# Performance work log

Hardware: AMD Instinct MI355X
Metric: run time of the kernel (lower is better)

Reference implementation:

```python
import jax, jax.numpy as jnp
import numpy as np

B, D, H, K = 32768, 784, 500, 50


def setup_inputs() -> dict:
    key = jax.random.key(0)
    ks = jax.random.split(key, 12)
    s = 0.02  # weight init scale
    return {
        "x": jax.random.uniform(ks[0], (B, D), dtype=jnp.float32),
        "u": jax.random.uniform(ks[1], (B, K), dtype=jnp.float32),
        "enc_w1": jax.random.normal(ks[2], (D, H), dtype=jnp.float32) * s,
        "enc_b1": jnp.zeros((H,), jnp.float32),
        "w_alpha": jax.random.normal(ks[3], (H, K), dtype=jnp.float32) * s,
        "b_alpha": jnp.zeros((K,), jnp.float32),
        "w_beta": jax.random.normal(ks[4], (H, K), dtype=jnp.float32) * s,
        "b_beta": jnp.zeros((K,), jnp.float32),
        "dec_w1": jax.random.normal(ks[5], (K, H), dtype=jnp.float32) * s,
        "dec_b1": jnp.zeros((H,), jnp.float32),
        "dec_w2": jax.random.normal(ks[6], (H, D), dtype=jnp.float32) * s,
        "dec_b2": jnp.zeros((D,), jnp.float32),
    }


def reference(x, u, enc_w1, enc_b1, w_alpha, b_alpha, w_beta, b_beta,
              dec_w1, dec_b1, dec_w2, dec_b2):
    # encode
    h = jax.nn.relu(x @ enc_w1 + enc_b1)                       # [B,H]
    alpha = jax.nn.softplus(h @ w_alpha + b_alpha)             # [B,K] > 0
    beta = jax.nn.softplus(h @ w_beta + b_beta)                # [B,K] > 0
    # Kumaraswamy inverse-CDF sample: v = (1 - u^(1/beta))^(1/alpha)
    v = (1.0 - u ** (1.0 / beta)) ** (1.0 / alpha)             # [B,K]
    # stick-breaking: pi[k] = v[k] * prod_{j<k}(1 - v[j])  (exclusive cumprod)
    cp = jnp.cumprod(1.0 - v, axis=-1)                         # [B,K]
    pi = v * jnp.concatenate([jnp.ones_like(v[:, :1]), cp[:, :-1]], axis=-1)
    # decode
    hd = jax.nn.relu(pi @ dec_w1 + dec_b1)                     # [B,H]
    recon_x = jax.nn.sigmoid(hd @ dec_w2 + dec_b2)             # [B,D]
    return recon_x, alpha, beta
```

## Files before the change

### kernel.cpp

```cpp
#include <hip/hip_runtime.h>
#include <math.h>


typedef __bf16 bf16x8 __attribute__((ext_vector_type(8)));
typedef float f32x4 __attribute__((ext_vector_type(4)));

#define BATCH 32768
#define BM 128
#define BN 128
#define BK 64
#define NTHR 512

__device__ __forceinline__ unsigned short bf16_bits(float f) {
    __bf16 b = (__bf16)f;
    return __builtin_bit_cast(unsigned short, b);
}

__device__ __forceinline__ void gll16(const void* src, void* ldsdst) {
    __builtin_amdgcn_global_load_lds(
        (const __attribute__((address_space(1))) unsigned int*)src,
        (__attribute__((address_space(3))) unsigned int*)ldsdst,
        16, 0, 0);
}

template<int MODE>
__global__ __launch_bounds__(NTHR, 4) void mfma_gemm(
    const unsigned short* __restrict__ A,
    const unsigned short* __restrict__ Bt,
    const float* __restrict__ bias,
    void* __restrict__ Cv,
    int Kpad, int lda, int ldc, int Nreal, int nbx)
{
    __shared__ unsigned short As[BM * BK];
    __shared__ unsigned short Bs[BN * BK];

    const int nwg = gridDim.x;
    const int orig = blockIdx.x;
    const int q = nwg >> 3, r8 = nwg & 7;
    const int xcd = orig & 7;
    const int chunkbase = (xcd < r8) ? xcd * (q + 1) : r8 * (q + 1) + (xcd - r8) * q;
    const int wgid = chunkbase + (orig >> 3);
    const int bn = wgid % nbx;
    const size_t block_m = (size_t)(wgid / nbx) * BM;
    const int block_n = bn * BN;

    const int tid = threadIdx.x;
    const int l = tid & 63;
    const int wid = tid >> 6;
    const int wr = wid >> 2, wc = wid & 3;

    const int lr = l & 15;
    const int kh = l >> 4;

    f32x4 acc[4][2] = {};

    for (int k0 = 0; k0 < Kpad; k0 += BK) {
        #pragma unroll
        for (int i = 0; i < 2; ++i) {
            int chunk = wid * 2 + i;
            int gid = chunk * 64 + l;
            int r = gid >> 3;
            int kgs = (gid & 7) ^ (r & 7);
            gll16(Bt + (size_t)(block_n + r) * Kpad + k0 + kgs * 8, Bs + chunk * 512);
        }
        #pragma unroll
        for (int i = 0; i < 2; ++i) {
            int chunk = wid * 2 + i;
            int gid = chunk * 64 + l;
            int r = gid >> 3;
            int kgs = (gid & 7) ^ (r & 7);
            gll16(A + (block_m + r) * (size_t)lda + k0 + kgs * 8, As + chunk * 512);
        }
        __syncthreads();

        #pragma unroll
        for (int s = 0; s < 2; ++s) {
            bf16x8 af[4], bf[2];
            #pragma unroll
            for (int mi = 0; mi < 4; ++mi) {
                int row = wr * 64 + mi * 16 + lr;
                int g = (s * 4 + kh) ^ (row & 7);
                af[mi] = *(const bf16x8*)(As + row * 64 + g * 8);
            }
            #pragma unroll
            for (int ni = 0; ni < 2; ++ni) {
                int row = wc * 32 + ni * 16 + lr;
                int g = (s * 4 + kh) ^ (row & 7);
                bf[ni] = *(const bf16x8*)(Bs + row * 64 + g * 8);
            }
            #pragma unroll
            for (int mi = 0; mi < 4; ++mi)
                #pragma unroll
                for (int ni = 0; ni < 2; ++ni)
                    acc[mi][ni] = __builtin_amdgcn_mfma_f32_16x16x32_bf16(
                        af[mi], bf[ni], acc[mi][ni], 0, 0, 0);
        }
        __syncthreads();
    }

    const int rg = (l >> 4) * 4;
    #pragma unroll
    for (int mi = 0; mi < 4; ++mi) {
        #pragma unroll
        for (int ni = 0; ni < 2; ++ni) {
            int gn = block_n + wc * 32 + ni * 16 + lr;
            float bs = bias[gn];
            #pragma unroll
            for (int j = 0; j < 4; ++j) {
                long gm = block_m + wr * 64 + mi * 16 + rg + j;
                float z = acc[mi][ni][j] + bs;
                if (MODE == 0) {
                    z = fmaxf(z, 0.f);
                    ((unsigned short*)Cv)[gm * ldc + gn] = bf16_bits(z);
                } else if (MODE == 1) {
                    z = (z > 0.f) ? z + __logf(1.f + __expf(-z))
                                  : __logf(1.f + __expf(z));
                    float* out = (float*)Cv;
                    if (gn < 50)       out[gm * 50 + gn] = z;
                    else if (gn < 100) out[(size_t)BATCH * 50 + gm * 50 + (gn - 50)] = z;
                } else {
                    if (gn < Nreal) {
                        z = __fdividef(1.f, 1.f + __expf(-z));
                        ((float*)Cv)[gm * Nreal + gn] = z;
                    }
                }
            }
        }
    }
}

__global__ __launch_bounds__(256) void cast_x(
    const float* __restrict__ x, unsigned short* __restrict__ xb)
{
    int gid = blockIdx.x * 256 + threadIdx.x;
    int r = gid / 104;
    int c = gid - r * 104;
    union { __bf16 b[8]; uint4 u; } pk;
    if (c < 98) {
        const float4* p = (const float4*)(x + (size_t)r * 784 + c * 8);
        float4 f0 = p[0], f1 = p[1];
        pk.b[0] = (__bf16)f0.x; pk.b[1] = (__bf16)f0.y;
        pk.b[2] = (__bf16)f0.z; pk.b[3] = (__bf16)f0.w;
        pk.b[4] = (__bf16)f1.x; pk.b[5] = (__bf16)f1.y;
        pk.b[6] = (__bf16)f1.z; pk.b[7] = (__bf16)f1.w;
    } else {
        pk.u = make_uint4(0, 0, 0, 0);
    }
    *(uint4*)(xb + (size_t)r * 832 + c * 8) = pk.u;
}

__global__ __launch_bounds__(256) void prep_bt(
    const float* __restrict__ W, const float* __restrict__ bias,
    unsigned short* __restrict__ Bt, float* __restrict__ bpad,
    int Kr, int Nr, int Kpad, int Npad)
{
    int idx = blockIdx.x * 256 + threadIdx.x;
    if (idx >= Npad * Kpad) return;
    int n = idx / Kpad, k = idx - n * Kpad;
    float v = (n < Nr && k < Kr) ? W[(size_t)k * Nr + n] : 0.f;
    Bt[idx] = bf16_bits(v);
    if (k == 0) bpad[n] = (n < Nr) ? bias[n] : 0.f;
}

__global__ __launch_bounds__(256) void prep_wab(
    const float* __restrict__ Wa, const float* __restrict__ Wb,
    const float* __restrict__ ba, const float* __restrict__ bb,
    unsigned short* __restrict__ Bt, float* __restrict__ bpad)
{
    int idx = blockIdx.x * 256 + threadIdx.x;
    if (idx >= 128 * 512) return;
    int n = idx >> 9, k = idx & 511;
    float v = 0.f;
    if (k < 500) {
        if (n < 50)       v = Wa[(size_t)k * 50 + n];
        else if (n < 100) v = Wb[(size_t)k * 50 + (n - 50)];
    }
    Bt[idx] = bf16_bits(v);
    if (k == 0) bpad[n] = (n < 50) ? ba[n] : ((n < 100) ? bb[n - 50] : 0.f);
}

__global__ __launch_bounds__(256) void sample_pi(
    const float* __restrict__ u, const float* __restrict__ alpha,
    const float* __restrict__ beta, unsigned short* __restrict__ pib)
{
    int row = (blockIdx.x * 256 + threadIdx.x) >> 6;
    int lane = threadIdx.x & 63;
    size_t base = (size_t)row * 50;

    float v = 0.f, w = 1.f;
    if (lane < 50) {
        float a = alpha[base + lane];
        float b = beta[base + lane];
        float uu = u[base + lane];
        float t = exp2f(__fdividef(log2f(uu), b));
        v = exp2f(__fdividef(log2f(1.f - t), a));
        w = 1.f - v;
    }
    float p = w;
    #pragma unroll
    for (int off = 1; off < 64; off <<= 1) {
        float t = __shfl_up(p, off, 64);
        if (lane >= off) p *= t;
    }
    float ex = __shfl_up(p, 1, 64);
    if (lane == 0) ex = 1.f;
    float pi = v * ex;
    pib[(size_t)row * 64 + lane] = (lane < 50) ? bf16_bits(pi) : (unsigned short)0;
}

extern "C" void kernel_launch(void* const* d_in, const int* in_sizes, int n_in,
                              void* d_out, int out_size, void* d_ws, size_t ws_size,
                              hipStream_t stream) {
    const float* x       = (const float*)d_in[0];
    const float* u       = (const float*)d_in[1];
    const float* enc_w1  = (const float*)d_in[2];
    const float* enc_b1  = (const float*)d_in[3];
    const float* w_alpha = (const float*)d_in[4];
    const float* b_alpha = (const float*)d_in[5];
    const float* w_beta  = (const float*)d_in[6];
    const float* b_beta  = (const float*)d_in[7];
    const float* dec_w1  = (const float*)d_in[8];
    const float* dec_b1  = (const float*)d_in[9];
    const float* dec_w2  = (const float*)d_in[10];
    const float* dec_b2  = (const float*)d_in[11];

    const int D = 784;

    float* out   = (float*)d_out;
    float* recon = out;
    float* alpha = out + (size_t)BATCH * D;

    unsigned short* xb = (unsigned short*)d_out;

    char* ws = (char*)d_ws;
    unsigned short* w1b  = (unsigned short*)(ws);
    unsigned short* wab  = (unsigned short*)(ws + 851968);
    unsigned short* dw1b = (unsigned short*)(ws + 983040);
    unsigned short* dw2b = (unsigned short*)(ws + 1048576);
    float* bias1  = (float*)(ws + 1966080);
    float* biasab = (float*)(ws + 1968128);
    float* biasd1 = (float*)(ws + 1970688);
    float* biasd2 = (float*)(ws + 1972736);
    unsigned short* h    = (unsigned short*)(ws + 2097152);
    unsigned short* pib  = (unsigned short*)(ws + 35651584);
    unsigned short* hdb  = h;

    cast_x<<<dim3(BATCH * 104 / 256), 256, 0, stream>>>(x, xb);
    prep_bt<<<dim3(512 * 832 / 256), 256, 0, stream>>>(
        enc_w1, enc_b1, w1b, bias1, 784, 500, 832, 512);
    prep_wab<<<dim3(256), 256, 0, stream>>>(w_alpha, w_beta, b_alpha, b_beta, wab, biasab);
    prep_bt<<<dim3(512 * 64 / 256), 256, 0, stream>>>(
        dec_w1, dec_b1, dw1b, biasd1, 50, 500, 64, 512);
    prep_bt<<<dim3(896 * 512 / 256), 256, 0, stream>>>(
        dec_w2, dec_b2, dw2b, biasd2, 500, 784, 512, 896);

    mfma_gemm<0><<<dim3((512 / BN) * (BATCH / BM)), NTHR, 0, stream>>>(
        xb, w1b, bias1, h, 832, 832, 512, 500, 512 / BN);

    mfma_gemm<1><<<dim3(BATCH / BM), NTHR, 0, stream>>>(
        h, wab, biasab, alpha, 512, 512, 0, 100, 1);

    sample_pi<<<dim3(BATCH * 64 / 256), 256, 0, stream>>>(
        u, alpha, alpha + (size_t)BATCH * 50, pib);

    mfma_gemm<0><<<dim3((512 / BN) * (BATCH / BM)), NTHR, 0, stream>>>(
        pib, dw1b, biasd1, hdb, 64, 64, 512, 500, 512 / BN);

    mfma_gemm<2><<<dim3((896 / BN) * (BATCH / BM)), NTHR, 0, stream>>>(
        hdb, dw2b, biasd2, recon, 512, 512, 784, 784, 896 / BN);
}
```

Measured before the change: 153.1 us.

## Fuse stick-breaking sampling into decoder first GEMM and merge weight-prep kernels

Adds a kernel that computes the Kumaraswamy samples and stick-breaking pi for a 128-row tile directly into LDS, then runs the 50→500 decoder GEMM with MFMA from that LDS tile. Weight tiles are double-buffered through global_load_lds. This removes the pi round-trip through global memory and one kernel launch, and each block now covers all 512 output columns instead of computing pi once per column block. The four weight-prep launches are also merged into one kernel with block-range dispatch. The cost is a serial sampling phase of 16 rows per wave before any MFMA work starts, plus scattered 2-byte stores of hdb.

```diff
diff --git a/kernel.cpp b/kernel.cpp
--- a/kernel.cpp
+++ b/kernel.cpp
@@ -129,6 +129,115 @@
     }
 }
 
+__global__ __launch_bounds__(NTHR, 4) void sample_gemm4(
+    const float* __restrict__ u, const float* __restrict__ alpha,
+    const float* __restrict__ beta,
+    const unsigned short* __restrict__ dw1b,
+    const float* __restrict__ biasd1,
+    unsigned short* __restrict__ hdb)
+{
+    __shared__ unsigned short Pi[128 * 64];
+    __shared__ unsigned short Wd[2][128 * 64];
+
+    const int tid = threadIdx.x;
+    const int l = tid & 63;
+    const int wid = tid >> 6;
+
+    const int nwg = gridDim.x;
+    const int orig = blockIdx.x;
+    const int q = nwg >> 3, r8 = nwg & 7;
+    const int xcd = orig & 7;
+    const int chunkbase = (xcd < r8) ? xcd * (q + 1) : r8 * (q + 1) + (xcd - r8) * q;
+    const int wgid = chunkbase + (orig >> 3);
+    const size_t block_m = (size_t)wgid * 128;
+
+    auto stageW = [&](int j, int buf) {
+        #pragma unroll
+        for (int i = 0; i < 2; ++i) {
+            int chunk = wid * 2 + i;
+            int gid = chunk * 64 + l;
+            int r = gid >> 3;
+            int kgs = (gid & 7) ^ (r & 7);
+            gll16(dw1b + (size_t)(j * 128 + r) * 64 + kgs * 8,
+                  &Wd[buf][chunk * 512]);
+        }
+    };
+
+    stageW(0, 0);
+
+    for (int rr = 0; rr < 16; ++rr) {
+        int row = wid * 16 + rr;
+        size_t grow = block_m + row;
+        float v = 0.f, w = 1.f;
+        if (l < 50) {
+            float a = alpha[grow * 50 + l];
+            float b = beta[grow * 50 + l];
+            float uu = u[grow * 50 + l];
+            float t = exp2f(__fdividef(log2f(uu), b));
+            v = exp2f(__fdividef(log2f(1.f - t), a));
+            w = 1.f - v;
+        }
+        float p = w;
+        #pragma unroll
+        for (int off = 1; off < 64; off <<= 1) {
+            float t2 = __shfl_up(p, off, 64);
+            if (l >= off) p *= t2;
+        }
+        float ex = __shfl_up(p, 1, 64);
+        if (l == 0) ex = 1.f;
+        float pi = (l < 50) ? v * ex : 0.f;
+        Pi[row * 64 + (((l >> 3) ^ (row & 7)) << 3) + (l & 7)] = bf16_bits(pi);
+    }
+    __syncthreads();
+
+    const int lr = l & 15, kh = l >> 4;
+    const int wr = wid >> 2, wc = wid & 3;
+    const int rg = (l >> 4) * 4;
+
+    for (int j = 0; j < 4; ++j) {
+        if (j < 3) stageW(j + 1, (j + 1) & 1);
+        f32x4 acc[4][2] = {};
+        const unsigned short* W = Wd[j & 1];
+        #pragma unroll
+        for (int s = 0; s < 2; ++s) {
+            bf16x8 af[4], bf[2];
+            #pragma unroll
+            for (int mi = 0; mi < 4; ++mi) {
+                int row = wr * 64 + mi * 16 + lr;
+                int g = (s * 4 + kh) ^ (row & 7);
+                af[mi] = *(const bf16x8*)(Pi + row * 64 + g * 8);
+            }
+            #pragma unroll
+            for (int ni = 0; ni < 2; ++ni) {
+                int row = wc * 32 + ni * 16 + lr;
+                int g = (s * 4 + kh) ^ (row & 7);
+                bf[ni] = *(const bf16x8*)(W + row * 64 + g * 8);
+            }
+            #pragma unroll
+            for (int mi = 0; mi < 4; ++mi)
+                #pragma unroll
+                for (int ni = 0; ni < 2; ++ni)
+                    acc[mi][ni] = __builtin_amdgcn_mfma_f32_16x16x32_bf16(
+                        af[mi], bf[ni], acc[mi][ni], 0, 0, 0);
+        }
+        #pragma unroll
+        for (int mi = 0; mi < 4; ++mi) {
+            #pragma unroll
+            for (int ni = 0; ni < 2; ++ni) {
+                int gn = j * 128 + wc * 32 + ni * 16 + lr;
+                float bs = biasd1[gn];
+                #pragma unroll
+                for (int jj = 0; jj < 4; ++jj) {
+                    long gm = block_m + wr * 64 + mi * 16 + rg + jj;
+                    float z = fmaxf(acc[mi][ni][jj] + bs, 0.f);
+                    hdb[gm * 512 + gn] = bf16_bits(z);
+                }
+            }
+        }
+        __syncthreads();
+    }
+}
+
 __global__ __launch_bounds__(256) void cast_x(
     const float* __restrict__ x, unsigned short* __restrict__ xb)
 {
@@ -149,63 +258,48 @@
     *(uint4*)(xb + (size_t)r * 832 + c * 8) = pk.u;
 }
 
-__global__ __launch_bounds__(256) void prep_bt(
-    const float* __restrict__ W, const float* __restrict__ bias,
-    unsigned short* __restrict__ Bt, float* __restrict__ bpad,
-    int Kr, int Nr, int Kpad, int Npad)
+__global__ __launch_bounds__(256) void prep_all(
+    const float* __restrict__ enc_w1, const float* __restrict__ enc_b1,
+    const float* __restrict__ Wa, const float* __restrict__ ba,
+    const float* __restrict__ Wb, const float* __restrict__ bb,
+    const float* __restrict__ dec_w1, const float* __restrict__ dec_b1,
+    const float* __restrict__ dec_w2, const float* __restrict__ dec_b2,
+    unsigned short* __restrict__ w1b, float* __restrict__ bias1,
+    unsigned short* __restrict__ wab, float* __restrict__ biasab,
+    unsigned short* __restrict__ dw1b, float* __restrict__ biasd1,
+    unsigned short* __restrict__ dw2b, float* __restrict__ biasd2)
 {
-    int idx = blockIdx.x * 256 + threadIdx.x;
-    if (idx >= Npad * Kpad) return;
-    int n = idx / Kpad, k = idx - n * Kpad;
-    float v = (n < Nr && k < Kr) ? W[(size_t)k * Nr + n] : 0.f;
-    Bt[idx] = bf16_bits(v);
-    if (k == 0) bpad[n] = (n < Nr) ? bias[n] : 0.f;
-}
-
-__global__ __launch_bounds__(256) void prep_wab(
-    const float* __restrict__ Wa, const float* __restrict__ Wb,
-    const float* __restrict__ ba, const float* __restrict__ bb,
-    unsigned short* __restrict__ Bt, float* __restrict__ bpad)
-{
-    int idx = blockIdx.x * 256 + threadIdx.x;
-    if (idx >= 128 * 512) return;
-    int n = idx >> 9, k = idx & 511;
-    float v = 0.f;
-    if (k < 500) {
-        if (n < 50)       v = Wa[(size_t)k * 50 + n];
-        else if (n < 100) v = Wb[(size_t)k * 50 + (n - 50)];
-    }
-    Bt[idx] = bf16_bits(v);
-    if (k == 0) bpad[n] = (n < 50) ? ba[n] : ((n < 100) ? bb[n - 50] : 0.f);
-}
-
-__global__ __launch_bounds__(256) void sample_pi(
-    const float* __restrict__ u, const float* __restrict__ alpha,
-    const float* __restrict__ beta, unsigned short* __restrict__ pib)
-{
-    int row = (blockIdx.x * 256 + threadIdx.x) >> 6;
-    int lane = threadIdx.x & 63;
-    size_t base = (size_t)row * 50;
-
-    float v = 0.f, w = 1.f;
-    if (lane < 50) {
-        float a = alpha[base + lane];
-        float b = beta[base + lane];
-        float uu = u[base + lane];
-        float t = exp2f(__fdividef(log2f(uu), b));
-        v = exp2f(__fdividef(log2f(1.f - t), a));
-        w = 1.f - v;
-    }
-    float p = w;
-    #pragma unroll
-    for (int off = 1; off < 64; off <<= 1) {
-        float t = __shfl_up(p, off, 64);
-        if (lane >= off) p *= t;
-    }
-    float ex = __shfl_up(p, 1, 64);
-    if (lane == 0) ex = 1.f;
-    float pi = v * ex;
-    pib[(size_t)row * 64 + lane] = (lane < 50) ? bf16_bits(pi) : (unsigned short)0;
+    int bid = blockIdx.x;
+    int t = threadIdx.x;
+    if (bid < 1664) {
+        int idx = bid * 256 + t;
+        int n = idx / 832, k = idx - n * 832;
+        float v = (n < 500 && k < 784) ? enc_w1[(size_t)k * 500 + n] : 0.f;
+        w1b[idx] = bf16_bits(v);
+        if (k == 0) bias1[n] = (n < 500) ? enc_b1[n] : 0.f;
+    } else if (bid < 1920) {
+        int idx = (bid - 1664) * 256 + t;
+        int n = idx >> 9, k = idx & 511;
+        float v = 0.f;
+        if (k < 500) {
+            if (n < 50)       v = Wa[(size_t)k * 50 + n];
+            else if (n < 100) v = Wb[(size_t)k * 50 + (n - 50)];
+        }
+        wab[idx] = bf16_bits(v);
+        if (k == 0) biasab[n] = (n < 50) ? ba[n] : ((n < 100) ? bb[n - 50] : 0.f);
+    } else if (bid < 2048) {
+        int idx = (bid - 1920) * 256 + t;
+        int n = idx >> 6, k = idx & 63;
+        float v = (n < 500 && k < 50) ? dec_w1[(size_t)k * 500 + n] : 0.f;
+        dw1b[idx] = bf16_bits(v);
+        if (k == 0) biasd1[n] = (n < 500) ? dec_b1[n] : 0.f;
+    } else {
+        int idx = (bid - 2048) * 256 + t;
+        int n = idx >> 9, k = idx & 511;
+        float v = (n < 784 && k < 500) ? dec_w2[(size_t)k * 784 + n] : 0.f;
+        dw2b[idx] = bf16_bits(v);
+        if (k == 0) biasd2[n] = (n < 784) ? dec_b2[n] : 0.f;
+    }
 }
 
 extern "C" void kernel_launch(void* const* d_in, const int* in_sizes, int n_in,
@@ -242,17 +336,13 @@
     float* biasd1 = (float*)(ws + 1970688);
     float* biasd2 = (float*)(ws + 1972736);
     unsigned short* h    = (unsigned short*)(ws + 2097152);
-    unsigned short* pib  = (unsigned short*)(ws + 35651584);
     unsigned short* hdb  = h;
 
     cast_x<<<dim3(BATCH * 104 / 256), 256, 0, stream>>>(x, xb);
-    prep_bt<<<dim3(512 * 832 / 256), 256, 0, stream>>>(
-        enc_w1, enc_b1, w1b, bias1, 784, 500, 832, 512);
-    prep_wab<<<dim3(256), 256, 0, stream>>>(w_alpha, w_beta, b_alpha, b_beta, wab, biasab);
-    prep_bt<<<dim3(512 * 64 / 256), 256, 0, stream>>>(
-        dec_w1, dec_b1, dw1b, biasd1, 50, 500, 64, 512);
-    prep_bt<<<dim3(896 * 512 / 256), 256, 0, stream>>>(
-        dec_w2, dec_b2, dw2b, biasd2, 500, 784, 512, 896);
+    prep_all<<<dim3(3840), 256, 0, stream>>>(
+        enc_w1, enc_b1, w_alpha, b_alpha, w_beta, b_beta,
+        dec_w1, dec_b1, dec_w2, dec_b2,
+        w1b, bias1, wab, biasab, dw1b, biasd1, dw2b, biasd2);
 
     mfma_gemm<0><<<dim3((512 / BN) * (BATCH / BM)), NTHR, 0, stream>>>(
         xb, w1b, bias1, h, 832, 832, 512, 500, 512 / BN);
@@ -260,11 +350,8 @@
     mfma_gemm<1><<<dim3(BATCH / BM), NTHR, 0, stream>>>(
         h, wab, biasab, alpha, 512, 512, 0, 100, 1);
 
-    sample_pi<<<dim3(BATCH * 64 / 256), 256, 0, stream>>>(
-        u, alpha, alpha + (size_t)BATCH * 50, pib);
-
-    mfma_gemm<0><<<dim3((512 / BN) * (BATCH / BM)), NTHR, 0, stream>>>(
-        pib, dw1b, biasd1, hdb, 64, 64, 512, 500, 512 / BN);
+    sample_gemm4<<<dim3(BATCH / 128), NTHR, 0, stream>>>(
+        u, alpha, alpha + (size_t)BATCH * 50, dw1b, biasd1, hdb);
 
     mfma_gemm<2><<<dim3((896 / BN) * (BATCH / BM)), NTHR, 0, stream>>>(
         hdb, dw2b, biasd2, recon, 512, 512, 784, 784, 896 / BN);
```

Result: no change. 150.8 us (-1.5%).
